# Optimization experiments

Hardware: AMD Instinct MI355X
Metric: run time of the kernel (lower is better)

## Reference

```python
import jax, jax.numpy as jnp
import numpy as np

VOCAB, D, B, T = 32000, 1024, 4, 2048

def setup_inputs() -> dict:
    key = jax.random.key(0)
    ks = jax.random.split(key, 7)
    std = 0.01  # model initializes all weights with std=0.01
    return {
        "x": jax.random.randint(ks[0], (B, T), 0, VOCAB),
        "emb_w": jax.random.normal(ks[1], (VOCAB, D), jnp.float32) * std,
        "wq": jax.random.normal(ks[2], (D, D), jnp.float32) * std,
        "wk": jax.random.normal(ks[3], (D, D), jnp.float32) * std,
        "wv": jax.random.normal(ks[4], (D, D), jnp.float32) * std,
        "wo": jax.random.normal(ks[5], (D, D), jnp.float32) * std,
        "wout": jax.random.normal(ks[6], (VOCAB, D), jnp.float32) * std,
    }

def fhe_act(x):
    # polynomial activation: 0.1*x^2 + 0.1*x
    return x * x * 0.1 + x * 0.1

def reference(x, emb_w, wq, wk, wv, wo, wout):
    h = emb_w[x] * 0.01                                 # [B,T,D]
    q = (h @ wq.T) * 0.01                               # [B,T,D]
    k = (h @ wk.T) * 0.01                               # [B,T,D]
    v = (h @ wv.T) * 0.1                                # [B,T,D]
    attn = jnp.einsum('btd,bsd->bts', q, k) * 0.01      # [B,T,T] full (no causal mask)
    attn = fhe_act(attn)
    out = jnp.einsum('bts,bsd->btd', attn, v) * 0.01    # [B,T,D]
    out = (out @ wo.T) * 0.1                            # [B,T,D]
    logits = out @ wout.T                               # [B,T,VOCAB]
    return logits
```

## Files before the change

kernel.cpp:

```cpp
#include <hip/hip_runtime.h>


typedef __bf16 bf16_t;
typedef __bf16 bf16x8 __attribute__((ext_vector_type(8)));
typedef __bf16 bf16x4 __attribute__((ext_vector_type(4)));
typedef float  f32x4  __attribute__((ext_vector_type(4)));

#define VOCAB 32000
#define DIM   1024
#define BATCH 4
#define SEQ   2048
#define BT    (BATCH*SEQ)

__device__ __forceinline__ void gload_lds16(const void* g, void* l) {
    __builtin_amdgcn_global_load_lds(
        (const __attribute__((address_space(1))) void*)g,
        (__attribute__((address_space(3))) void*)l,
        16, 0, 0);
}

__global__ void cast_f32_to_bf16(const float* __restrict__ in, bf16_t* __restrict__ out, int n4) {
    int i = blockIdx.x * blockDim.x + threadIdx.x;
    if (i < n4) {
        float4 v = ((const float4*)in)[i];
        bf16x4 o;
        o.x = (bf16_t)v.x; o.y = (bf16_t)v.y; o.z = (bf16_t)v.z; o.w = (bf16_t)v.w;
        ((bf16x4*)out)[i] = o;
    }
}

__global__ void embed_gather(const int* __restrict__ x, const float* __restrict__ emb,
                             bf16_t* __restrict__ h) {
    const int tok = blockIdx.x;
    const int row = x[tok];
    const float4* src = (const float4*)(emb + (long)row * DIM);
    bf16x4* dst = (bf16x4*)(h + (long)tok * DIM);
    int j = threadIdx.x;
    float4 v = src[j];
    bf16x4 o;
    o.x = (bf16_t)(v.x * 0.01f); o.y = (bf16_t)(v.y * 0.01f);
    o.z = (bf16_t)(v.z * 0.01f); o.w = (bf16_t)(v.w * 0.01f);
    dst[j] = o;
}

template<int ACT, typename CT>
__global__ __launch_bounds__(256) void gemm_bt(
    const bf16_t* __restrict__ A, const bf16_t* __restrict__ B, CT* __restrict__ C,
    int M, int N, int K, long sA, long sB, long sC, float scale)
{
    __shared__ __align__(16) bf16_t lsA[128 * 32];
    __shared__ __align__(16) bf16_t lsB[128 * 32];

    const int bz = blockIdx.z;
    A += (long)bz * sA;  B += (long)bz * sB;  C += (long)bz * sC;

    const int tm = blockIdx.y, tn = blockIdx.x;
    const int t = threadIdx.x;
    const int lane = t & 63, wave = t >> 6;
    const int wm = (wave >> 1) * 64;
    const int wn = (wave & 1) * 64;

    const int srow = t >> 2;
    const int scol = (t & 3) * 8;
    const bf16_t* gA = A + (long)(tm * 128 + srow) * K + scol;
    const bf16_t* gB = B + (long)(tn * 128 + srow) * K + scol;
    bf16_t* lA = &lsA[srow * 32 + scol];
    bf16_t* lB = &lsB[srow * 32 + scol];

    f32x4 acc[4][4];
#pragma unroll
    for (int i = 0; i < 4; ++i)
#pragma unroll
        for (int j = 0; j < 4; ++j)
            acc[i][j] = (f32x4){0.f, 0.f, 0.f, 0.f};

    const int arow = lane & 15;
    const int acol = (lane >> 4) * 8;

    for (int k0 = 0; k0 < K; k0 += 32) {
        __syncthreads();
        gload_lds16(gA + k0,                lA);
        gload_lds16(gA + k0 + 64 * (long)K, lA + 64 * 32);
        gload_lds16(gB + k0,                lB);
        gload_lds16(gB + k0 + 64 * (long)K, lB + 64 * 32);
        __syncthreads();

        bf16x8 af[4], bfr[4];
#pragma unroll
        for (int i = 0; i < 4; ++i) {
            af[i]  = *(const bf16x8*)&lsA[(wm + i * 16 + arow) * 32 + acol];
            bfr[i] = *(const bf16x8*)&lsB[(wn + i * 16 + arow) * 32 + acol];
        }
#pragma unroll
        for (int i = 0; i < 4; ++i)
#pragma unroll
            for (int j = 0; j < 4; ++j)
                acc[i][j] = __builtin_amdgcn_mfma_f32_16x16x32_bf16(af[i], bfr[j], acc[i][j], 0, 0, 0);
    }

    const int crow0 = tm * 128 + wm + (lane >> 4) * 4;
    const int ccol0 = tn * 128 + wn + (lane & 15);
#pragma unroll
    for (int i = 0; i < 4; ++i)
#pragma unroll
        for (int j = 0; j < 4; ++j)
#pragma unroll
            for (int r = 0; r < 4; ++r) {
                float s = acc[i][j][r] * scale;
                if (ACT) s = s * s * 0.1f + s * 0.1f;
                C[(long)(crow0 + i * 16 + r) * N + (ccol0 + j * 16)] = (CT)s;
            }
}

__global__ __launch_bounds__(512, 2) void gemm_bt_256(
    const bf16_t* __restrict__ A, const bf16_t* __restrict__ B, float* __restrict__ C,
    int N, int K, float scale)
{
    __shared__ __align__(16) char smem[131072];
    char* const sm = smem;

    const int lin = blockIdx.x;
    const int xcd = lin & 7, jj = lin >> 3;
    const int tm = xcd * 4 + (jj & 3);
    const int tn = jj >> 2;
    const long trow0 = (long)tm * 256, tcol0 = (long)tn * 256;

    const int tid  = threadIdx.x;
    const int lane = tid & 63;
    const int wave = tid >> 6;
    const int wm = wave >> 2;
    const int wn = wave & 3;
    const int lr = lane & 15;
    const int ko2 = (lane >> 4) * 16;
    const int rbase = lr * 64 + (ko2 ^ (((lr >> 1) & 3) << 4));

    const int o0 = tid * 16, o1 = 8192 + tid * 16;
    int sr0, sc0, sr1, sc1;
    {
        int ol = o0 ^ (((o0 >> 7) & 3) << 4);
        sr0 = ((ol >> 10) >> 1) * 16 + ((ol >> 6) & 15);
        sc0 = ((ol >> 10) & 1) * 32 + ((ol & 63) >> 1);
        ol = o1 ^ (((o1 >> 7) & 3) << 4);
        sr1 = ((ol >> 10) >> 1) * 16 + ((ol >> 6) & 15);
        sc1 = ((ol >> 10) & 1) * 32 + ((ol & 63) >> 1);
    }

    const bf16_t* Abase = A + trow0 * K;
    const bf16_t* Bbase = B + tcol0 * K;

#define STAGE_HT(gbase, kt, half, ldsh) do {                                          \
    gload_lds16((gbase) + (long)((half) * 128 + sr0) * K + ((kt) * 64 + sc0), (ldsh) + o0); \
    gload_lds16((gbase) + (long)((half) * 128 + sr1) * K + ((kt) * 64 + sc1), (ldsh) + o1); \
} while (0)

    f32x4 acc[8][4];
#pragma unroll
    for (int i = 0; i < 8; ++i)
#pragma unroll
        for (int j = 0; j < 4; ++j)
            acc[i][j] = (f32x4){0.f, 0.f, 0.f, 0.f};

#define PHASE_LO(ks, ...) do {                                                        \
    bf16x8 af_[4];                                                                    \
    af_[0] = *(const bf16x8*)(ldsA + ((wm * 4 + 0) * 2 + (ks)) * 1024 + rbase);       \
    _Pragma("unroll")                                                                 \
    for (int c_ = 0; c_ < 4; ++c_)                                                    \
        bv_[c_] = *(const bf16x8*)(ldsB + (c_ >> 1) * 16384 +                         \
                      ((wn * 2 + (c_ & 1)) * 2 + (ks)) * 1024 + rbase);               \
    _Pragma("unroll")                                                                 \
    for (int i_ = 1; i_ < 4; ++i_)                                                    \
        af_[i_] = *(const bf16x8*)(ldsA +                                             \
                      ((wm * 4 + i_) * 2 + (ks)) * 1024 + rbase);                     \
    __VA_ARGS__;                                                                      \
    __builtin_amdgcn_s_setprio(1);                                                    \
    _Pragma("unroll")                                                                 \
    for (int i_ = 0; i_ < 4; ++i_)                                                    \
        _Pragma("unroll")                                                             \
        for (int c_ = 0; c_ < 4; ++c_)                                                \
            acc[i_][c_] = __builtin_amdgcn_mfma_f32_16x16x32_bf16(                    \
                af_[i_], bv_[c_], acc[i_][c_], 0, 0, 0);                              \
    __builtin_amdgcn_s_setprio(0);                                                    \
    __builtin_amdgcn_sched_barrier(0);                                                \
    asm volatile("s_barrier" ::: "memory");                                           \
} while (0)

#define PHASE_HI(ks, ...) do {                                                        \
    bf16x8 af_[4];                                                                    \
    _Pragma("unroll")                                                                 \
    for (int i_ = 0; i_ < 4; ++i_)                                                    \
        af_[i_] = *(const bf16x8*)(ldsA + 16384 +                                     \
                      ((wm * 4 + i_) * 2 + (ks)) * 1024 + rbase);                     \
    __VA_ARGS__;                                                                      \
    __builtin_amdgcn_s_setprio(1);                                                    \
    _Pragma("unroll")                                                                 \
    for (int i_ = 0; i_ < 4; ++i_)                                                    \
        _Pragma("unroll")                                                             \
        for (int c_ = 0; c_ < 4; ++c_)                                                \
            acc[4 + i_][c_] = __builtin_amdgcn_mfma_f32_16x16x32_bf16(                \
                af_[i_], bv_[c_], acc[4 + i_][c_], 0, 0, 0);                          \
    __builtin_amdgcn_s_setprio(0);                                                    \
    __builtin_amdgcn_sched_barrier(0);                                                \
} while (0)

    {
        char* a0 = sm;
        char* b0 = sm + 32768;
        char* a1 = sm + 65536;
        char* b1 = sm + 65536 + 32768;
        STAGE_HT(Abase, 0, 0, a0);
        STAGE_HT(Bbase, 0, 0, b0);
        STAGE_HT(Abase, 0, 1, a0 + 16384);
        STAGE_HT(Bbase, 0, 1, b0 + 16384);
        STAGE_HT(Abase, 1, 0, a1);
        STAGE_HT(Bbase, 1, 0, b1);
        asm volatile("s_waitcnt vmcnt(4)" ::: "memory");
        asm volatile("s_barrier" ::: "memory");
    }

    const int NT = K / 64;
    for (int t = 0; t < NT; ++t) {
        const int buf = t & 1;
        char* ldsA  = sm + buf * 65536;
        char* ldsB  = ldsA + 32768;
        char* ldsAn = sm + (buf ^ 1) * 65536;
        char* ldsBn = ldsAn + 32768;
        bf16x8 bv_[4];

        PHASE_LO(0,
              if (t + 1 < NT) {
                  STAGE_HT(Abase, t + 1, 1, ldsAn + 16384);
                  STAGE_HT(Bbase, t + 1, 1, ldsBn + 16384);
              });

        PHASE_HI(0, );
        asm volatile("s_barrier" ::: "memory");

        PHASE_LO(1, );

        PHASE_HI(1,
              if (t + 2 < NT) {
                  STAGE_HT(Abase, t + 2, 0, ldsA);
                  STAGE_HT(Bbase, t + 2, 0, ldsB);
              });
        if (t + 2 < NT) { asm volatile("s_waitcnt vmcnt(4)" ::: "memory"); }
        else            { asm volatile("s_waitcnt vmcnt(0)" ::: "memory"); }
        asm volatile("s_barrier" ::: "memory");
    }

    const int erow = (lane >> 4) * 4;
    const int ecol = lane & 15;
#pragma unroll
    for (int a = 0; a < 8; ++a)
#pragma unroll
        for (int c = 0; c < 4; ++c)
#pragma unroll
            for (int r = 0; r < 4; ++r) {
                long row = trow0 + (a >> 2) * 128 + wm * 64 + (a & 3) * 16 + erow + r;
                long col = tcol0 + (c >> 1) * 128 + wn * 32 + (c & 1) * 16 + ecol;
                C[row * N + col] = acc[a][c][r] * scale;
            }
#undef PHASE_LO
#undef PHASE_HI
#undef STAGE_HT
}

extern "C" void kernel_launch(void* const* d_in, const int* in_sizes, int n_in,
                              void* d_out, int out_size, void* d_ws, size_t ws_size,
                              hipStream_t stream) {
    const int*   x    = (const int*)d_in[0];
    const float* emb  = (const float*)d_in[1];
    const float* wq   = (const float*)d_in[2];
    const float* wk   = (const float*)d_in[3];
    const float* wv   = (const float*)d_in[4];
    const float* wo   = (const float*)d_in[5];
    const float* wout = (const float*)d_in[6];
    float* logits = (float*)d_out;

    char* ws = (char*)d_ws;
    size_t off = 0;
    auto alloc = [&](size_t bytes) {
        char* p = ws + off;
        off += (bytes + 255) & ~(size_t)255;
        return p;
    };
    bf16_t* hb    = (bf16_t*)alloc((size_t)BT * DIM * 2);
    bf16_t* qb    = (bf16_t*)alloc((size_t)BT * DIM * 2);
    bf16_t* kb    = (bf16_t*)alloc((size_t)BT * DIM * 2);
    bf16_t* vtb   = (bf16_t*)alloc((size_t)BATCH * DIM * SEQ * 2);
    bf16_t* attnb = (bf16_t*)alloc((size_t)BATCH * SEQ * SEQ * 2);
    bf16_t* o1b   = (bf16_t*)alloc((size_t)BT * DIM * 2);
    bf16_t* o2b   = (bf16_t*)alloc((size_t)BT * DIM * 2);
    bf16_t* wqb   = (bf16_t*)alloc((size_t)DIM * DIM * 2);
    bf16_t* wkb   = (bf16_t*)alloc((size_t)DIM * DIM * 2);
    bf16_t* wvb   = (bf16_t*)alloc((size_t)DIM * DIM * 2);
    bf16_t* wob   = (bf16_t*)alloc((size_t)DIM * DIM * 2);
    bf16_t* woutb = (bf16_t*)alloc((size_t)VOCAB * DIM * 2);

    {
        int n4 = DIM * DIM / 4;
        cast_f32_to_bf16<<<n4 / 256, 256, 0, stream>>>(wq, wqb, n4);
        cast_f32_to_bf16<<<n4 / 256, 256, 0, stream>>>(wk, wkb, n4);
        cast_f32_to_bf16<<<n4 / 256, 256, 0, stream>>>(wv, wvb, n4);
        cast_f32_to_bf16<<<n4 / 256, 256, 0, stream>>>(wo, wob, n4);
        int n4o = VOCAB * DIM / 4;
        cast_f32_to_bf16<<<n4o / 256, 256, 0, stream>>>(wout, woutb, n4o);
    }

    embed_gather<<<BT, 256, 0, stream>>>(x, emb, hb);

    dim3 blk(256);
    gemm_bt<0, bf16_t><<<dim3(DIM / 128, BT / 128, 1), blk, 0, stream>>>(
        hb, wqb, qb, BT, DIM, DIM, 0, 0, 0, 0.01f);
    gemm_bt<0, bf16_t><<<dim3(DIM / 128, BT / 128, 1), blk, 0, stream>>>(
        hb, wkb, kb, BT, DIM, DIM, 0, 0, 0, 0.01f);
    gemm_bt<0, bf16_t><<<dim3(SEQ / 128, DIM / 128, BATCH), blk, 0, stream>>>(
        wvb, hb, vtb, DIM, SEQ, DIM, 0, (long)SEQ * DIM, (long)DIM * SEQ, 0.1f);
    gemm_bt<1, bf16_t><<<dim3(SEQ / 128, SEQ / 128, BATCH), blk, 0, stream>>>(
        qb, kb, attnb, SEQ, SEQ, DIM,
        (long)SEQ * DIM, (long)SEQ * DIM, (long)SEQ * SEQ, 0.01f);
    gemm_bt<0, bf16_t><<<dim3(DIM / 128, SEQ / 128, BATCH), blk, 0, stream>>>(
        attnb, vtb, o1b, SEQ, DIM, SEQ,
        (long)SEQ * SEQ, (long)DIM * SEQ, (long)SEQ * DIM, 0.01f);
    gemm_bt<0, bf16_t><<<dim3(DIM / 128, BT / 128, 1), blk, 0, stream>>>(
        o1b, wob, o2b, BT, DIM, DIM, 0, 0, 0, 0.1f);

    gemm_bt_256<<<(BT / 256) * (VOCAB / 256), 512, 0, stream>>>(
        o2b, woutb, logits, VOCAB, DIM, 1.0f);
}
```

Before: 937.4 us.

## Software-pipeline LDS fragment loads with double-buffered registers across GEMM phases

Restructures the main GEMM loop so the A and B fragments for the next phase are read from LDS into a second register set while the current phase's MFMAs run, including prefetching the next tile's first fragments before the end-of-iteration barrier. The global-to-LDS staging order and the vmcnt waits are rearranged so the B upper half is loaded together with the lower halves. This aims to hide LDS read latency behind MFMA work. In exchange it uses more VGPRs, which may lower occupancy or cause spills, and the hand-set waitcnt and barrier placement leaves a risk of LDS races.

```diff
diff --git a/kernel.cpp b/kernel.cpp
--- a/kernel.cpp
+++ b/kernel.cpp
@@ -160,47 +160,32 @@
         for (int j = 0; j < 4; ++j)
             acc[i][j] = (f32x4){0.f, 0.f, 0.f, 0.f};
 
-#define PHASE_LO(ks, ...) do {                                                        \
-    bf16x8 af_[4];                                                                    \
-    af_[0] = *(const bf16x8*)(ldsA + ((wm * 4 + 0) * 2 + (ks)) * 1024 + rbase);       \
+    bf16x8 af0[4], af1[4], bv0[4], bv1[4];
+
+#define LD_A(dst, base, h, ks) do {                                                   \
+    _Pragma("unroll")                                                                 \
+    for (int i_ = 0; i_ < 4; ++i_)                                                    \
+        dst[i_] = *(const bf16x8*)((base) + (h) * 16384 +                             \
+                      ((wm * 4 + i_) * 2 + (ks)) * 1024 + rbase);                     \
+} while (0)
+#define LD_B(dst, base, ks) do {                                                      \
     _Pragma("unroll")                                                                 \
     for (int c_ = 0; c_ < 4; ++c_)                                                    \
-        bv_[c_] = *(const bf16x8*)(ldsB + (c_ >> 1) * 16384 +                         \
+        dst[c_] = *(const bf16x8*)((base) + (c_ >> 1) * 16384 +                       \
                       ((wn * 2 + (c_ & 1)) * 2 + (ks)) * 1024 + rbase);               \
-    _Pragma("unroll")                                                                 \
-    for (int i_ = 1; i_ < 4; ++i_)                                                    \
-        af_[i_] = *(const bf16x8*)(ldsA +                                             \
-                      ((wm * 4 + i_) * 2 + (ks)) * 1024 + rbase);                     \
-    __VA_ARGS__;                                                                      \
+} while (0)
+#define MFMA16(r0, af, bv) do {                                                       \
     __builtin_amdgcn_s_setprio(1);                                                    \
     _Pragma("unroll")                                                                 \
     for (int i_ = 0; i_ < 4; ++i_)                                                    \
         _Pragma("unroll")                                                             \
         for (int c_ = 0; c_ < 4; ++c_)                                                \
-            acc[i_][c_] = __builtin_amdgcn_mfma_f32_16x16x32_bf16(                    \
-                af_[i_], bv_[c_], acc[i_][c_], 0, 0, 0);                              \
-    __builtin_amdgcn_s_setprio(0);                                                    \
-    __builtin_amdgcn_sched_barrier(0);                                                \
-    asm volatile("s_barrier" ::: "memory");                                           \
-} while (0)
-
-#define PHASE_HI(ks, ...) do {                                                        \
-    bf16x8 af_[4];                                                                    \
-    _Pragma("unroll")                                                                 \
-    for (int i_ = 0; i_ < 4; ++i_)                                                    \
-        af_[i_] = *(const bf16x8*)(ldsA + 16384 +                                     \
-                      ((wm * 4 + i_) * 2 + (ks)) * 1024 + rbase);                     \
-    __VA_ARGS__;                                                                      \
-    __builtin_amdgcn_s_setprio(1);                                                    \
-    _Pragma("unroll")                                                                 \
-    for (int i_ = 0; i_ < 4; ++i_)                                                    \
-        _Pragma("unroll")                                                             \
-        for (int c_ = 0; c_ < 4; ++c_)                                                \
-            acc[4 + i_][c_] = __builtin_amdgcn_mfma_f32_16x16x32_bf16(                \
-                af_[i_], bv_[c_], acc[4 + i_][c_], 0, 0, 0);                          \
+            acc[(r0) + i_][c_] = __builtin_amdgcn_mfma_f32_16x16x32_bf16(             \
+                af[i_], bv[c_], acc[(r0) + i_][c_], 0, 0, 0);                         \
     __builtin_amdgcn_s_setprio(0);                                                    \
     __builtin_amdgcn_sched_barrier(0);                                                \
 } while (0)
+#define BAR() asm volatile("s_barrier" ::: "memory")
 
     {
         char* a0 = sm;
@@ -208,43 +193,55 @@
         char* a1 = sm + 65536;
         char* b1 = sm + 65536 + 32768;
         STAGE_HT(Abase, 0, 0, a0);
+        STAGE_HT(Abase, 0, 1, a0 + 16384);
         STAGE_HT(Bbase, 0, 0, b0);
-        STAGE_HT(Abase, 0, 1, a0 + 16384);
         STAGE_HT(Bbase, 0, 1, b0 + 16384);
         STAGE_HT(Abase, 1, 0, a1);
         STAGE_HT(Bbase, 1, 0, b1);
-        asm volatile("s_waitcnt vmcnt(4)" ::: "memory");
-        asm volatile("s_barrier" ::: "memory");
+        STAGE_HT(Bbase, 1, 1, b1 + 16384);
+        asm volatile("s_waitcnt vmcnt(6)" ::: "memory");
+        BAR();
+        LD_A(af0, sm, 0, 0);
+        LD_B(bv0, sm + 32768, 0);
     }
 
     const int NT = K / 64;
     for (int t = 0; t < NT; ++t) {
-        const int buf = t & 1;
-        char* ldsA  = sm + buf * 65536;
+        char* ldsA  = sm + (t & 1) * 65536;
         char* ldsB  = ldsA + 32768;
-        char* ldsAn = sm + (buf ^ 1) * 65536;
+        char* ldsAn = sm + ((t & 1) ^ 1) * 65536;
         char* ldsBn = ldsAn + 32768;
-        bf16x8 bv_[4];
-
-        PHASE_LO(0,
-              if (t + 1 < NT) {
-                  STAGE_HT(Abase, t + 1, 1, ldsAn + 16384);
-                  STAGE_HT(Bbase, t + 1, 1, ldsBn + 16384);
-              });
-
-        PHASE_HI(0, );
-        asm volatile("s_barrier" ::: "memory");
-
-        PHASE_LO(1, );
-
-        PHASE_HI(1,
-              if (t + 2 < NT) {
-                  STAGE_HT(Abase, t + 2, 0, ldsA);
-                  STAGE_HT(Bbase, t + 2, 0, ldsB);
-              });
-        if (t + 2 < NT) { asm volatile("s_waitcnt vmcnt(4)" ::: "memory"); }
-        else            { asm volatile("s_waitcnt vmcnt(0)" ::: "memory"); }
-        asm volatile("s_barrier" ::: "memory");
+
+        LD_A(af1, ldsA, 1, 0);
+        if (t + 1 < NT) STAGE_HT(Abase, t + 1, 1, ldsAn + 16384);
+        MFMA16(0, af0, bv0);
+        BAR();
+
+        LD_A(af0, ldsA, 0, 1);
+        LD_B(bv1, ldsB, 1);
+        MFMA16(4, af1, bv0);
+        BAR();
+
+        LD_A(af1, ldsA, 1, 1);
+        MFMA16(0, af0, bv1);
+        asm volatile("s_waitcnt vmcnt(2)" ::: "memory");
+        BAR();
+
+        if (t + 1 < NT) {
+            LD_A(af0, ldsAn, 0, 0);
+            LD_B(bv0, ldsBn, 0);
+        }
+        if (t + 2 < NT) {
+            STAGE_HT(Abase, t + 2, 0, ldsA);
+            STAGE_HT(Bbase, t + 2, 0, ldsB);
+            STAGE_HT(Bbase, t + 2, 1, ldsB + 16384);
+            MFMA16(4, af1, bv1);
+            asm volatile("s_waitcnt vmcnt(6)" ::: "memory");
+        } else {
+            MFMA16(4, af1, bv1);
+            asm volatile("s_waitcnt vmcnt(0)" ::: "memory");
+        }
+        BAR();
     }
 
     const int erow = (lane >> 4) * 4;
@@ -259,8 +256,10 @@
                 long col = tcol0 + (c >> 1) * 128 + wn * 32 + (c & 1) * 16 + ecol;
                 C[row * N + col] = acc[a][c][r] * scale;
             }
-#undef PHASE_LO
-#undef PHASE_HI
+#undef LD_A
+#undef LD_B
+#undef MFMA16
+#undef BAR
 #undef STAGE_HT
 }
 
```

New measurement: 1.767 ms. 88.5% more time.
